# Optimization experiments

Hardware: AMD Instinct MI355X
Metric: run time of the kernel (lower is better)

Reference implementation:

```python
import jax, jax.numpy as jnp
import numpy as np

REG_MAX = 16
NC = 80
TOPK = 10
ALPHA = 0.5
BETA = 6.0
IMG = 640.0
EPS = 1e-7
BOX_W, CLS_W, DFL_W = 7.5, 0.5, 1.5


def make_anchors():
    anchors, strides = [], []
    for s, size in [(8, 80), (16, 40), (32, 20)]:
        yy, xx = jnp.meshgrid(jnp.arange(size, dtype=jnp.float32), jnp.arange(size, dtype=jnp.float32), indexing='ij')
        xy = (jnp.stack([xx, yy], -1).reshape(-1, 2) + 0.5) * s
        anchors.append(xy)
        strides.append(jnp.full((size * size,), float(s), jnp.float32))
    return jnp.concatenate(anchors), jnp.concatenate(strides)  # [A,2], [A]


def pairwise_iou(gt, pd, eps=EPS):
    # gt [B,G,4], pd [B,A,4] -> [B,G,A]
    b1 = gt[:, :, None, :]
    b2 = pd[:, None, :, :]
    inter = jnp.clip(jnp.minimum(b1[..., 2:], b2[..., 2:]) - jnp.maximum(b1[..., :2], b2[..., :2]), 0.0).prod(-1)
    a1 = (b1[..., 2:] - b1[..., :2]).prod(-1)
    a2 = (b2[..., 2:] - b2[..., :2]).prod(-1)
    return inter / (a1 + a2 - inter + eps)


def ciou(b1, b2, eps=EPS):
    # elementwise CIoU on [...,4] xyxy boxes
    inter = jnp.clip(jnp.minimum(b1[..., 2:], b2[..., 2:]) - jnp.maximum(b1[..., :2], b2[..., :2]), 0.0).prod(-1)
    area1 = jnp.maximum(b1[..., 2:] - b1[..., :2], eps).prod(-1)
    area2 = jnp.maximum(b2[..., 2:] - b2[..., :2], eps).prod(-1)
    union = area1 + area2 - inter + eps
    iou = inter / union
    cw = jnp.maximum(b1[..., 2], b2[..., 2]) - jnp.minimum(b1[..., 0], b2[..., 0])
    ch = jnp.maximum(b1[..., 3], b2[..., 3]) - jnp.minimum(b1[..., 1], b2[..., 1])
    c2 = cw * cw + ch * ch + eps
    c1c = (b1[..., :2] + b1[..., 2:]) * 0.5
    c2c = (b2[..., :2] + b2[..., 2:]) * 0.5
    rho2 = ((c1c - c2c) ** 2).sum(-1)
    w1 = jnp.maximum(b1[..., 2] - b1[..., 0], eps)
    h1 = jnp.maximum(b1[..., 3] - b1[..., 1], eps)
    w2 = jnp.maximum(b2[..., 2] - b2[..., 0], eps)
    h2 = jnp.maximum(b2[..., 3] - b2[..., 1], eps)
    v = (4.0 / jnp.pi ** 2) * (jnp.arctan(w2 / h2) - jnp.arctan(w1 / h1)) ** 2
    alpha = jax.lax.stop_gradient(v / (1.0 - iou + v + eps))
    return jnp.clip(iou - (rho2 / c2 + v * alpha), -1.0, 1.0)


def assign(pd_scores, pd_bboxes, gt_labels, gt_bboxes, mask_gt_f):
    # TaskAlignedAssigner.forward (runs under stop_gradient at call site)
    B, A, C = pd_scores.shape
    G = gt_bboxes.shape[1]
    iou = pairwise_iou(gt_bboxes, pd_bboxes)                       # [B,G,A]
    cls_score = pd_scores.max(-1)[:, None, :] * mask_gt_f[:, :, None]
    align = (cls_score ** ALPHA) * (iou ** BETA) * mask_gt_f[:, :, None]
    k = min(TOPK, A)
    vals, idx = jax.lax.top_k(align, k)                            # [B,G,k]
    valid = (mask_gt_f[:, :, None] > 0) & (vals > 0)
    b_ix = jnp.arange(B)[:, None, None]
    g_ix = jnp.arange(G)[None, :, None]
    mask_pos = jnp.zeros((B, G, A), bool).at[b_ix, g_ix, idx].max(valid)
    fg = mask_pos.any(1)                                           # [B,A]
    miou = iou * mask_pos.astype(iou.dtype)
    matched = miou.argmax(1)                                       # [B,A]
    tlab = jnp.take_along_axis(gt_labels, matched, 1)
    tlab = jnp.clip(tlab, 0, C - 1)
    tlab = jnp.where(fg, tlab, 0)
    tbox = jnp.take_along_axis(gt_bboxes, matched[..., None], 1)   # [B,A,4]
    iou_s = jnp.take_along_axis(miou, matched[:, None, :], 1)[:, 0, :]
    tscore = jax.nn.one_hot(tlab, C, dtype=pd_scores.dtype) * iou_s[..., None] * fg[..., None].astype(pd_scores.dtype)
    return tlab, tbox, tscore, fg


def yolo_loss(pred_dist, pred_cls, gt_labels, gt_bboxes, mask_gt):
    B, A, _ = pred_dist.shape
    R = REG_MAX
    anchors, strides = make_anchors()
    # decode: DFL expectation -> pixel boxes
    prob = jax.nn.softmax(pred_dist.reshape(B, A, 4, R), -1)
    dist = (prob * jnp.arange(R, dtype=prob.dtype)).sum(-1)        # stride units
    dpix = dist * strides[None, :, None]
    ax, ay = anchors[None, :, 0], anchors[None, :, 1]
    pred_boxes = jnp.clip(jnp.stack([ax - dpix[..., 0], ay - dpix[..., 1], ax + dpix[..., 2], ay + dpix[..., 3]], -1), 0.0, IMG)
    pd_scores = jax.nn.sigmoid(pred_cls)
    mgf = mask_gt.astype(jnp.float32)
    tlab, tbox, tscore, fg = jax.tree.map(jax.lax.stop_gradient, assign(pd_scores, pred_boxes, gt_labels, gt_bboxes, mgf))
    # cls: BCE with logits, sum / max(score_sum, 1)
    x, t = pred_cls, tscore
    bce = jnp.maximum(x, 0.0) - x * t + jnp.log1p(jnp.exp(-jnp.abs(x)))
    score_sum = jnp.maximum(tscore.sum(), 1.0)
    loss_cls = bce.sum() / score_sum
    fgf = fg.astype(jnp.float32)
    num_fg = jnp.maximum(fgf.sum(), 1.0)
    # box: mean(1 - CIoU) over foreground anchors
    loss_box = ((1.0 - ciou(pred_boxes, tbox)) * fgf).sum() / num_fg
    # DFL: box2dist in stride units, bilinear CE over left/right bins
    target_ltrb = jnp.stack([ax - tbox[..., 0], ay - tbox[..., 1], tbox[..., 2] - ax, tbox[..., 3] - ay], -1) / strides[None, :, None]
    target_ltrb = jnp.clip(target_ltrb, 0.0, R - 1.01)
    tleft = jnp.clip(jnp.floor(target_ltrb).astype(jnp.int32), 0, R - 1)
    tright = jnp.clip(tleft + 1, 0, R - 1)
    wr = jnp.clip(target_ltrb - tleft.astype(target_ltrb.dtype), 0.0, 1.0)
    wl = 1.0 - wr
    logp = jax.nn.log_softmax(pred_dist.reshape(B, A, 4, R), -1)
    ll = -jnp.take_along_axis(logp, tleft[..., None], -1)[..., 0]
    lr = -jnp.take_along_axis(logp, tright[..., None], -1)[..., 0]
    dfl = (ll * wl + lr * wr).sum(-1)                              # [B,A]
    loss_dfl = (dfl * fgf).sum() / num_fg / 4.0
    return BOX_W * loss_box + CLS_W * loss_cls + DFL_W * loss_dfl


def setup_inputs() -> dict:
    key = jax.random.key(0)
    k0, k1, k2, k3, k4 = jax.random.split(key, 5)
    B, A, G = 32, 8400, 40
    pred_dist = jax.random.normal(k0, (B, A, 4 * REG_MAX), dtype=jnp.float32)
    pred_cls = jax.random.normal(k1, (B, A, NC), dtype=jnp.float32)
    gt_labels = jax.random.randint(k2, (B, G), 0, NC)
    centers = jax.random.uniform(k3, (B, G, 2), minval=60.0, maxval=580.0)
    wh = jax.random.uniform(k4, (B, G, 2), minval=10.0, maxval=100.0)
    gt_bboxes = jnp.concatenate([centers - wh * 0.5, centers + wh * 0.5], -1).astype(jnp.float32)
    mask_gt = jnp.ones((B, G), dtype=bool)
    return {"pred_dist": pred_dist, "pred_cls": pred_cls, "gt_labels": gt_labels, "gt_bboxes": gt_bboxes, "mask_gt": mask_gt}


def reference(pred_dist, pred_cls, gt_labels, gt_bboxes, mask_gt):
    return yolo_loss(pred_dist, pred_cls, gt_labels, gt_bboxes, mask_gt)
```

## Files before the change

### kernel.cpp

```cpp
#include <hip/hip_runtime.h>
#include <cmath>


namespace {

constexpr int B = 32;
constexpr int A = 8400;
constexpr int G = 40;
constexpr int C = 80;
constexpr float EPS = 1e-7f;
constexpr float IMG = 640.0f;

constexpr int TPW = 16;
constexpr int NT = B * A / TPW;
constexpr int PRE_BLOCKS = 512;
constexpr int NWAVES = PRE_BLOCKS * 4;
constexpr int DIST_B = TPW * 64;
constexpr int CLS_B = TPW * 320;
constexpr int SLICE = DIST_B + CLS_B;

#define AS1 __attribute__((address_space(1)))
#define AS3 __attribute__((address_space(3)))

__device__ __forceinline__ void gload_lds16(const void* g, void* l) {
  __builtin_amdgcn_global_load_lds((AS1 void*)(g), (AS3 void*)(l), 16, 0, 0);
}

__device__ __forceinline__ void anchor_of(int a, float& ax, float& ay, float& st) {
  int x, y;
  if (a < 6400)      { x = a % 80; y = a / 80; st = 8.0f; }
  else if (a < 8000) { int t = a - 6400; x = t % 40; y = t / 40; st = 16.0f; }
  else               { int t = a - 8000; x = t % 20; y = t / 20; st = 32.0f; }
  ax = ((float)x + 0.5f) * st;
  ay = ((float)y + 0.5f) * st;
}

__device__ __forceinline__ void cls_part(const float4* c, float& sp, float& mx) {
  float relu = 0.f, p0 = 1.f, p1 = 1.f;
  mx = -3.4e38f;
#pragma unroll
  for (int q = 0; q < 5; ++q) {
    float xs[4] = {c[q].x, c[q].y, c[q].z, c[q].w};
#pragma unroll
    for (int e = 0; e < 4; ++e) {
      float x = xs[e];
      mx = fmaxf(mx, x);
      relu += fmaxf(x, 0.f);
      float ee = __expf(-fabsf(x));
      if (q < 3) p0 *= (1.f + ee); else p1 *= (1.f + ee);
    }
  }
  sp = relu + 0.69314718056f * (__log2f(p0) + __log2f(p1));
}

__device__ __forceinline__ float dist_expect(float4 w0, float4 w1, float4 w2, float4 w3) {
  float x[16] = {w0.x, w0.y, w0.z, w0.w, w1.x, w1.y, w1.z, w1.w,
                 w2.x, w2.y, w2.z, w2.w, w3.x, w3.y, w3.z, w3.w};
  float m = x[0];
#pragma unroll
  for (int e = 1; e < 16; ++e) m = fmaxf(m, x[e]);
  float se = 0.f, sj = 0.f;
#pragma unroll
  for (int e = 0; e < 16; ++e) {
    float ee = __expf(x[e] - m);
    se += ee;
    sj += ee * (float)e;
  }
  return sj / se;
}

__device__ __forceinline__ void stage_tile(const char* dbase, const char* cbase,
                                           int tile, char* lbuf, int lane) {
  const char* gd = dbase + (size_t)tile * DIST_B + lane * 16;
  const char* gc = cbase + (size_t)tile * CLS_B + lane * 16;
#pragma unroll
  for (int r = 0; r < 4; ++r) gload_lds16(gd + r * 1024, lbuf + r * 1024);
#pragma unroll
  for (int q = 0; q < 5; ++q) gload_lds16(gc + q * 1024, lbuf + DIST_B + q * 1024);
}

__global__ __launch_bounds__(256) void k_pre(
    const float* __restrict__ pred_dist, const float* __restrict__ pred_cls,
    float* __restrict__ pbox, float* __restrict__ msqrt,
    unsigned long long* __restrict__ mask, double* __restrict__ acc) {
  __shared__ char smem[4 * 2 * SLICE];
  __shared__ double shb[4];
  int t = threadIdx.x, lane = t & 63, wid = t >> 6;
  int j = lane & 3, a16 = lane >> 2;
  char* slice = smem + wid * (2 * SLICE);
  const char* dbase = (const char*)pred_dist;
  const char* cbase = (const char*)pred_cls;

  double spsum = 0.0;
  int cur = blockIdx.x * 4 + wid;
  int buf = 0;
  if (cur < NT) stage_tile(dbase, cbase, cur, slice, lane);

  while (cur < NT) {
    int nxt = cur + NWAVES;
    if (nxt < NT) {
      stage_tile(dbase, cbase, nxt, slice + (buf ^ 1) * SLICE, lane);
      __builtin_amdgcn_s_waitcnt(0xF79);
    } else {
      __builtin_amdgcn_s_waitcnt(0xF70);
    }

    const char* bp = slice + buf * SLICE;
    float4 c[5];
    const float4* cl = (const float4*)(bp + DIST_B + a16 * 320 + j * 16);
#pragma unroll
    for (int q = 0; q < 5; ++q) c[q] = cl[q * 4];
    float sp, mx;
    cls_part(c, sp, mx);
    mx = fmaxf(mx, __shfl_xor(mx, 1));
    mx = fmaxf(mx, __shfl_xor(mx, 2));

    const float4* dl = (const float4*)(bp + a16 * 256 + j * 64);
    float de = dist_expect(dl[0], dl[1], dl[2], dl[3]);
    int qb = lane & ~3;
    float e0 = __shfl(de, qb), e1 = __shfl(de, qb + 1);
    float e2 = __shfl(de, qb + 2), e3 = __shfl(de, qb + 3);

    int i = cur * TPW + a16;
    if (j == 0) {
      int a = i % A;
      float ax, ay, st;
      anchor_of(a, ax, ay, st);
      float4 ob;
      ob.x = fminf(fmaxf(ax - e0 * st, 0.f), IMG);
      ob.y = fminf(fmaxf(ay - e1 * st, 0.f), IMG);
      ob.z = fminf(fmaxf(ax + e2 * st, 0.f), IMG);
      ob.w = fminf(fmaxf(ay + e3 * st, 0.f), IMG);
      reinterpret_cast<float4*>(pbox)[i] = ob;
      msqrt[i] = sqrtf(1.f / (1.f + __expf(-mx)));
      mask[i] = 0ull;
    }
    spsum += (double)sp;
    cur = nxt;
    buf ^= 1;
  }

#pragma unroll
  for (int off = 32; off; off >>= 1) spsum += __shfl_xor(spsum, off);
  if (lane == 0) shb[wid] = spsum;
  __syncthreads();
  if (t == 0) {
    double s = shb[0] + shb[1] + shb[2] + shb[3];
    atomicAdd(&acc[0 * 8 + (blockIdx.x & 7)], s);
  }
}

__global__ __launch_bounds__(256) void k_topk(
    const float* __restrict__ pbox, const float* __restrict__ msqrt,
    const float* __restrict__ gt_bboxes, unsigned long long* __restrict__ mask) {
  int bg = blockIdx.x;
  int b = bg / G, g = bg % G;
  int t = threadIdx.x, lane = t & 63, wid = t >> 6;
  const float* gp = gt_bboxes + (size_t)bg * 4;
  float gx1 = gp[0], gy1 = gp[1], gx2 = gp[2], gy2 = gp[3];
  float garea = (gx2 - gx1) * (gy2 - gy1);
  const float4* pb = reinterpret_cast<const float4*>(pbox) + (size_t)b * A;
  const float* ms = msqrt + (size_t)b * A;

  float lv[10];
  int li[10];
#pragma unroll
  for (int s = 0; s < 10; ++s) { lv[s] = 0.f; li[s] = 0x7fffffff; }

  for (int a = t; a < A; a += 256) {
    float4 p = pb[a];
    float iw = fmaxf(fminf(gx2, p.z) - fmaxf(gx1, p.x), 0.f);
    float ih = fmaxf(fminf(gy2, p.w) - fmaxf(gy1, p.y), 0.f);
    float inter = iw * ih;
    float parea = (p.z - p.x) * (p.w - p.y);
    float iou = inter / (garea + parea - inter + EPS);
    float i2 = iou * iou;
    float v = ms[a] * i2 * i2 * i2;
    if (v > lv[9] || (v == lv[9] && v > 0.f && a < li[9])) {
      float cv = v; int ci = a;
#pragma unroll
      for (int s = 0; s < 10; ++s) {
        bool bt = (cv > lv[s]) || (cv == lv[s] && ci < li[s]);
        float tv = bt ? cv : lv[s]; int ti = bt ? ci : li[s];
        cv = bt ? lv[s] : cv; ci = bt ? li[s] : ci;
        lv[s] = tv; li[s] = ti;
      }
    }
  }

  __shared__ float swv[4];
  __shared__ int swi[4];
  __shared__ float sbv;
  __shared__ int sbi;
  int ptr = 0;
  unsigned long long* mrow = mask + (size_t)b * A;
  for (int k = 0; k < 10; ++k) {
    float hv = lv[0]; int hi = li[0];
#pragma unroll
    for (int s = 1; s < 10; ++s) { bool sel = (ptr == s); hv = sel ? lv[s] : hv; hi = sel ? li[s] : hi; }
    if (ptr > 9) { hv = -1.f; hi = -1; }
    float rv = hv; int ri = hi;
#pragma unroll
    for (int off = 32; off; off >>= 1) {
      float ov = __shfl_xor(rv, off); int oi = __shfl_xor(ri, off);
      if (ov > rv || (ov == rv && oi < ri)) { rv = ov; ri = oi; }
    }
    if (lane == 0) { swv[wid] = rv; swi[wid] = ri; }
    __syncthreads();
    if (t == 0) {
      float bv = swv[0]; int bi = swi[0];
#pragma unroll
      for (int w = 1; w < 4; ++w)
        if (swv[w] > bv || (swv[w] == bv && swi[w] < bi)) { bv = swv[w]; bi = swi[w]; }
      sbv = bv; sbi = bi;
      if (bv > 0.f) atomicOr(&mrow[bi], 1ull << g);
    }
    __syncthreads();
    if (sbv <= 0.f) break;
    if (hi == sbi) ptr++;
  }
}

__device__ __forceinline__ float ciou_f(float4 p, float t0, float t1, float t2, float t3) {
  float iw = fmaxf(fminf(p.z, t2) - fmaxf(p.x, t0), 0.f);
  float ih = fmaxf(fminf(p.w, t3) - fmaxf(p.y, t1), 0.f);
  float inter = iw * ih;
  float w1 = fmaxf(p.z - p.x, EPS), h1 = fmaxf(p.w - p.y, EPS);
  float w2 = fmaxf(t2 - t0, EPS), h2 = fmaxf(t3 - t1, EPS);
  float uni = w1 * h1 + w2 * h2 - inter + EPS;
  float iou = inter / uni;
  float cw = fmaxf(p.z, t2) - fminf(p.x, t0);
  float ch = fmaxf(p.w, t3) - fminf(p.y, t1);
  float c2 = cw * cw + ch * ch + EPS;
  float dx = (p.x + p.z) * 0.5f - (t0 + t2) * 0.5f;
  float dy = (p.y + p.w) * 0.5f - (t1 + t3) * 0.5f;
  float rho2 = dx * dx + dy * dy;
  float dat = atanf(w2 / h2) - atanf(w1 / h1);
  const float c4pi2 = (float)(4.0 / (M_PI * M_PI));
  float v = c4pi2 * dat * dat;
  float alpha = v / (1.0f - iou + v + EPS);
  float r = iou - (rho2 / c2 + v * alpha);
  return fminf(fmaxf(r, -1.f), 1.f);
}

__device__ __forceinline__ float wave_sum(float v) {
#pragma unroll
  for (int off = 32; off; off >>= 1) v += __shfl_xor(v, off);
  return v;
}

__global__ __launch_bounds__(256) void k_loss(
    const float* __restrict__ pred_dist, const float* __restrict__ pred_cls,
    const int* __restrict__ gt_labels, const float* __restrict__ gt_bboxes,
    const float* __restrict__ pbox, const unsigned long long* __restrict__ mask,
    double* __restrict__ acc) {
  int t = threadIdx.x, lane = t & 63, wid = t >> 6;
  int i = blockIdx.x * 256 + t;
  int b = i / A, a = i - b * A;
  unsigned long long mk = mask[i];
  float corr = 0.f, sc = 0.f, nfg = 0.f, box = 0.f, dfl = 0.f;
  if (mk) {
    float4 p = reinterpret_cast<const float4*>(pbox)[i];
    float parea = (p.z - p.x) * (p.w - p.y);
    float best = 0.f;
    int bestg = -1;
    unsigned long long mm = mk;
    while (mm) {
      int g = __ffsll((unsigned long long)mm) - 1;
      mm &= mm - 1;
      const float* gp = gt_bboxes + (size_t)(b * G + g) * 4;
      float gx1 = gp[0], gy1 = gp[1], gx2 = gp[2], gy2 = gp[3];
      float iw = fmaxf(fminf(gx2, p.z) - fmaxf(gx1, p.x), 0.f);
      float ih = fmaxf(fminf(gy2, p.w) - fmaxf(gy1, p.y), 0.f);
      float inter = iw * ih;
      float garea = (gx2 - gx1) * (gy2 - gy1);
      float iou = inter / (garea + parea - inter + EPS);
      if (iou > best) { best = iou; bestg = g; }
    }
    if (bestg >= 0) {
      sc = best;
      nfg = 1.f;
      int lab = gt_labels[b * G + bestg];
      lab = lab < 0 ? 0 : (lab > C - 1 ? C - 1 : lab);
      float xl = pred_cls[(size_t)i * C + lab];
      corr = -xl * best;
      const float* gp = gt_bboxes + (size_t)(b * G + bestg) * 4;
      float t0 = gp[0], t1 = gp[1], t2 = gp[2], t3 = gp[3];
      box = 1.0f - ciou_f(p, t0, t1, t2, t3);
      float ax, ay, st;
      anchor_of(a, ax, ay, st);
      float rst = 1.f / st;
      float tgt[4] = {(ax - t0) * rst, (ay - t1) * rst, (t2 - ax) * rst, (t3 - ay) * rst};
      const float4* dr = reinterpret_cast<const float4*>(pred_dist) + (size_t)i * 16;
      const float* drf = pred_dist + (size_t)i * 64;
#pragma unroll
      for (int l = 0; l < 4; ++l) {
        float4 u0 = dr[4 * l], u1 = dr[4 * l + 1], u2 = dr[4 * l + 2], u3 = dr[4 * l + 3];
        float xs[16] = {u0.x, u0.y, u0.z, u0.w, u1.x, u1.y, u1.z, u1.w,
                        u2.x, u2.y, u2.z, u2.w, u3.x, u3.y, u3.z, u3.w};
        float m = xs[0];
#pragma unroll
        for (int e = 1; e < 16; ++e) m = fmaxf(m, xs[e]);
        float se = 0.f;
#pragma unroll
        for (int e = 0; e < 16; ++e) se += __expf(xs[e] - m);
        float lse = m + __logf(se);
        float tt = fminf(fmaxf(tgt[l], 0.f), 14.99f);
        int tl = (int)tt;
        float wr = tt - (float)tl;
        float wl = 1.f - wr;
        float xa = drf[l * 16 + tl];
        float xb = drf[l * 16 + tl + 1];
        dfl += (lse - xa) * wl + (lse - xb) * wr;
      }
    }
  }
  float s0 = wave_sum(corr), s1 = wave_sum(sc), s2 = wave_sum(nfg);
  float s3 = wave_sum(box), s4 = wave_sum(dfl);
  __shared__ float sh[4][5];
  if (lane == 0) { sh[wid][0] = s0; sh[wid][1] = s1; sh[wid][2] = s2; sh[wid][3] = s3; sh[wid][4] = s4; }
  __syncthreads();
  if (t == 0) {
    double a0 = 0, a1 = 0, a2 = 0, a3 = 0, a4 = 0;
#pragma unroll
    for (int w = 0; w < 4; ++w) {
      a0 += sh[w][0]; a1 += sh[w][1]; a2 += sh[w][2]; a3 += sh[w][3]; a4 += sh[w][4];
    }
    if (a2 != 0.0) {
      int slot = blockIdx.x & 7;
      atomicAdd(&acc[0 * 8 + slot], a0);
      atomicAdd(&acc[1 * 8 + slot], a1);
      atomicAdd(&acc[2 * 8 + slot], a2);
      atomicAdd(&acc[3 * 8 + slot], a3);
      atomicAdd(&acc[4 * 8 + slot], a4);
    }
  }
}

__global__ void k_final(const double* __restrict__ acc, float* __restrict__ out) {
  double q[5];
#pragma unroll
  for (int jj = 0; jj < 5; ++jj) {
    double s = 0;
#pragma unroll
    for (int w = 0; w < 8; ++w) s += acc[jj * 8 + w];
    q[jj] = s;
  }
  double bce = q[0];
  double scs = fmax(q[1], 1.0);
  double nf = fmax(q[2], 1.0);
  double loss = 7.5 * (q[3] / nf) + 0.5 * (bce / scs) + 1.5 * (q[4] / nf / 4.0);
  out[0] = (float)loss;
}

}

extern "C" void kernel_launch(void* const* d_in, const int* in_sizes, int n_in,
                              void* d_out, int out_size, void* d_ws, size_t ws_size,
                              hipStream_t stream) {
  (void)in_sizes; (void)n_in; (void)out_size; (void)ws_size;
  const float* pred_dist = (const float*)d_in[0];
  const float* pred_cls  = (const float*)d_in[1];
  const int*   gt_labels = (const int*)d_in[2];
  const float* gt_bboxes = (const float*)d_in[3];

  unsigned long long* mask = (unsigned long long*)d_ws;
  double* acc  = (double*)((char*)d_ws + (size_t)B * A * 8);
  float*  pbox = (float*)((char*)d_ws + (size_t)B * A * 8 + 64 * 8);
  float*  msqrt = pbox + (size_t)B * A * 4;
  float*  out = (float*)d_out;

  hipMemsetAsync(acc, 0, 64 * 8, stream);
  hipLaunchKernelGGL(k_pre, dim3(PRE_BLOCKS), dim3(256), 0, stream,
                     pred_dist, pred_cls, pbox, msqrt, mask, acc);
  hipLaunchKernelGGL(k_topk, dim3(B * G), dim3(256), 0, stream,
                     pbox, msqrt, gt_bboxes, mask);
  hipLaunchKernelGGL(k_loss, dim3(B * A / 256), dim3(256), 0, stream,
                     pred_dist, pred_cls, gt_labels, gt_bboxes, pbox, mask, acc);
  hipLaunchKernelGGL(k_final, dim3(1), dim3(1), 0, stream, acc, out);
}
```

Measured before the change: 239.8 us.

## Split top-k into candidate compaction and per-wave top-10 selection

The per-(batch,gt) top-k kernel, which scanned all 8400 anchors per block, is replaced by two kernels. The first computes IoU-based scores for all gts per anchor and appends only positive-score candidates to per-gt lists via atomics. The second selects the top 10 from each compacted list using one wave per gt with no block-level syncs. The distribution-expectation loop in the pre kernel also rotates its LDS float4 read order by anchor, apparently to avoid bank conflicts. The change adds atomic contention and a capped candidate buffer, and candidates beyond the cap are silently dropped.

After: 679.9 us. 2.84x slower.

```diff
diff --git a/kernel.cpp b/kernel.cpp
--- a/kernel.cpp
+++ b/kernel.cpp
@@ -19,6 +19,8 @@
 constexpr int CLS_B = TPW * 320;
 constexpr int SLICE = DIST_B + CLS_B;
 
+constexpr int CAP = 6144;
+
 #define AS1 __attribute__((address_space(1)))
 #define AS3 __attribute__((address_space(3)))
 
@@ -51,22 +53,6 @@
     }
   }
   sp = relu + 0.69314718056f * (__log2f(p0) + __log2f(p1));
-}
-
-__device__ __forceinline__ float dist_expect(float4 w0, float4 w1, float4 w2, float4 w3) {
-  float x[16] = {w0.x, w0.y, w0.z, w0.w, w1.x, w1.y, w1.z, w1.w,
-                 w2.x, w2.y, w2.z, w2.w, w3.x, w3.y, w3.z, w3.w};
-  float m = x[0];
-#pragma unroll
-  for (int e = 1; e < 16; ++e) m = fmaxf(m, x[e]);
-  float se = 0.f, sj = 0.f;
-#pragma unroll
-  for (int e = 0; e < 16; ++e) {
-    float ee = __expf(x[e] - m);
-    se += ee;
-    sj += ee * (float)e;
-  }
-  return sj / se;
 }
 
 __device__ __forceinline__ void stage_tile(const char* dbase, const char* cbase,
@@ -115,8 +101,31 @@
     mx = fmaxf(mx, __shfl_xor(mx, 1));
     mx = fmaxf(mx, __shfl_xor(mx, 2));
 
-    const float4* dl = (const float4*)(bp + a16 * 256 + j * 64);
-    float de = dist_expect(dl[0], dl[1], dl[2], dl[3]);
+    const char* dlb = bp + a16 * 256 + j * 64;
+    int rot = a16 & 3;
+    float4 dd[4];
+    float b4[4];
+#pragma unroll
+    for (int r = 0; r < 4; ++r) {
+      int cc = (r + rot) & 3;
+      dd[r] = *(const float4*)(dlb + cc * 16);
+      b4[r] = (float)(4 * cc);
+    }
+    float m = dd[0].x;
+#pragma unroll
+    for (int r = 0; r < 4; ++r) {
+      m = fmaxf(m, dd[r].x); m = fmaxf(m, dd[r].y);
+      m = fmaxf(m, dd[r].z); m = fmaxf(m, dd[r].w);
+    }
+    float se = 0.f, sj = 0.f;
+#pragma unroll
+    for (int r = 0; r < 4; ++r) {
+      float e0 = __expf(dd[r].x - m), e1 = __expf(dd[r].y - m);
+      float e2 = __expf(dd[r].z - m), e3 = __expf(dd[r].w - m);
+      se += e0 + e1 + e2 + e3;
+      sj += e0 * b4[r] + e1 * (b4[r] + 1.f) + e2 * (b4[r] + 2.f) + e3 * (b4[r] + 3.f);
+    }
+    float de = sj / se;
     int qb = lane & ~3;
     float e0 = __shfl(de, qb), e1 = __shfl(de, qb + 1);
     float e2 = __shfl(de, qb + 2), e3 = __shfl(de, qb + 3);
@@ -150,32 +159,58 @@
   }
 }
 
-__global__ __launch_bounds__(256) void k_topk(
+__global__ __launch_bounds__(256) void k_cand(
     const float* __restrict__ pbox, const float* __restrict__ msqrt,
-    const float* __restrict__ gt_bboxes, unsigned long long* __restrict__ mask) {
-  int bg = blockIdx.x;
+    const float* __restrict__ gt_bboxes,
+    int* __restrict__ cnt, int2* __restrict__ cand) {
+  int b = blockIdx.x >> 3, chunk = blockIdx.x & 7;
+  __shared__ float4 sgt[G];
+  if (threadIdx.x < G) sgt[threadIdx.x] = ((const float4*)gt_bboxes)[b * G + threadIdx.x];
+  __syncthreads();
+  const float4* pb = (const float4*)pbox + (size_t)b * A;
+  const float* ms = msqrt + (size_t)b * A;
+  for (int idx = threadIdx.x; idx < 1050; idx += 256) {
+    int a = chunk * 1050 + idx;
+    float4 p = pb[a];
+    float parea = (p.z - p.x) * (p.w - p.y);
+    float m = ms[a];
+    for (int g = 0; g < G; ++g) {
+      float4 gb = sgt[g];
+      float iw = fmaxf(fminf(gb.z, p.z) - fmaxf(gb.x, p.x), 0.f);
+      float ih = fmaxf(fminf(gb.w, p.w) - fmaxf(gb.y, p.y), 0.f);
+      float inter = iw * ih;
+      float garea = (gb.z - gb.x) * (gb.w - gb.y);
+      float iou = inter / (garea + parea - inter + EPS);
+      float i2 = iou * iou;
+      float v = m * i2 * i2 * i2;
+      if (v > 0.f) {
+        int bg = b * G + g;
+        int pos = atomicAdd(&cnt[bg], 1);
+        if (pos < CAP) cand[(size_t)bg * CAP + pos] = make_int2(__float_as_int(v), a);
+      }
+    }
+  }
+}
+
+__global__ __launch_bounds__(256) void k_top10(
+    const int* __restrict__ cnt, const int2* __restrict__ cand,
+    unsigned long long* __restrict__ mask) {
+  int lane = threadIdx.x & 63, wid = threadIdx.x >> 6;
+  int bg = blockIdx.x * 4 + wid;
   int b = bg / G, g = bg % G;
-  int t = threadIdx.x, lane = t & 63, wid = t >> 6;
-  const float* gp = gt_bboxes + (size_t)bg * 4;
-  float gx1 = gp[0], gy1 = gp[1], gx2 = gp[2], gy2 = gp[3];
-  float garea = (gx2 - gx1) * (gy2 - gy1);
-  const float4* pb = reinterpret_cast<const float4*>(pbox) + (size_t)b * A;
-  const float* ms = msqrt + (size_t)b * A;
+  int n = cnt[bg];
+  if (n > CAP) n = CAP;
+  const int2* cc = cand + (size_t)bg * CAP;
 
   float lv[10];
   int li[10];
 #pragma unroll
   for (int s = 0; s < 10; ++s) { lv[s] = 0.f; li[s] = 0x7fffffff; }
 
-  for (int a = t; a < A; a += 256) {
-    float4 p = pb[a];
-    float iw = fmaxf(fminf(gx2, p.z) - fmaxf(gx1, p.x), 0.f);
-    float ih = fmaxf(fminf(gy2, p.w) - fmaxf(gy1, p.y), 0.f);
-    float inter = iw * ih;
-    float parea = (p.z - p.x) * (p.w - p.y);
-    float iou = inter / (garea + parea - inter + EPS);
-    float i2 = iou * iou;
-    float v = ms[a] * i2 * i2 * i2;
+  for (int e = lane; e < n; e += 64) {
+    int2 en = cc[e];
+    float v = __int_as_float(en.x);
+    int a = en.y;
     if (v > lv[9] || (v == lv[9] && v > 0.f && a < li[9])) {
       float cv = v; int ci = a;
 #pragma unroll
@@ -188,12 +223,8 @@
     }
   }
 
-  __shared__ float swv[4];
-  __shared__ int swi[4];
-  __shared__ float sbv;
-  __shared__ int sbi;
+  unsigned long long* mrow = mask + (size_t)b * A;
   int ptr = 0;
-  unsigned long long* mrow = mask + (size_t)b * A;
   for (int k = 0; k < 10; ++k) {
     float hv = lv[0]; int hi = li[0];
 #pragma unroll
@@ -205,19 +236,9 @@
       float ov = __shfl_xor(rv, off); int oi = __shfl_xor(ri, off);
       if (ov > rv || (ov == rv && oi < ri)) { rv = ov; ri = oi; }
     }
-    if (lane == 0) { swv[wid] = rv; swi[wid] = ri; }
-    __syncthreads();
-    if (t == 0) {
-      float bv = swv[0]; int bi = swi[0];
-#pragma unroll
-      for (int w = 1; w < 4; ++w)
-        if (swv[w] > bv || (swv[w] == bv && swi[w] < bi)) { bv = swv[w]; bi = swi[w]; }
-      sbv = bv; sbi = bi;
-      if (bv > 0.f) atomicOr(&mrow[bi], 1ull << g);
-    }
-    __syncthreads();
-    if (sbv <= 0.f) break;
-    if (hi == sbi) ptr++;
+    if (rv <= 0.f) break;
+    if (lane == 0) atomicOr(&mrow[ri], 1ull << g);
+    if (hi == ri) ptr++;
   }
 }
 
@@ -364,17 +385,23 @@
   const int*   gt_labels = (const int*)d_in[2];
   const float* gt_bboxes = (const float*)d_in[3];
 
-  unsigned long long* mask = (unsigned long long*)d_ws;
-  double* acc  = (double*)((char*)d_ws + (size_t)B * A * 8);
-  float*  pbox = (float*)((char*)d_ws + (size_t)B * A * 8 + 64 * 8);
-  float*  msqrt = pbox + (size_t)B * A * 4;
-  float*  out = (float*)d_out;
-
-  hipMemsetAsync(acc, 0, 64 * 8, stream);
+  char* ws = (char*)d_ws;
+  unsigned long long* mask = (unsigned long long*)ws;
+  size_t off = (size_t)B * A * 8;
+  double* acc = (double*)(ws + off);       off += 64 * 8;
+  int* cnt    = (int*)(ws + off);          off += (size_t)B * G * 4;
+  int2* cand  = (int2*)(ws + off);         off += (size_t)B * G * CAP * 8;
+  float* pbox = (float*)(ws + off);        off += (size_t)B * A * 16;
+  float* msqrt = (float*)(ws + off);
+  float* out = (float*)d_out;
+
+  hipMemsetAsync(acc, 0, 64 * 8 + (size_t)B * G * 4, stream);
   hipLaunchKernelGGL(k_pre, dim3(PRE_BLOCKS), dim3(256), 0, stream,
                      pred_dist, pred_cls, pbox, msqrt, mask, acc);
-  hipLaunchKernelGGL(k_topk, dim3(B * G), dim3(256), 0, stream,
-                     pbox, msqrt, gt_bboxes, mask);
+  hipLaunchKernelGGL(k_cand, dim3(B * 8), dim3(256), 0, stream,
+                     pbox, msqrt, gt_bboxes, cnt, cand);
+  hipLaunchKernelGGL(k_top10, dim3(B * G / 4), dim3(256), 0, stream,
+                     cnt, cand, mask);
   hipLaunchKernelGGL(k_loss, dim3(B * A / 256), dim3(256), 0, stream,
                      pred_dist, pred_cls, gt_labels, gt_bboxes, pbox, mask, acc);
   hipLaunchKernelGGL(k_final, dim3(1), dim3(1), 0, stream, acc, out);
```
